# Kernel optimization log

Hardware: AMD Instinct MI355X
Metric: run time of the kernel (lower is better)

## Reference

```python
import jax, jax.numpy as jnp
import numpy as np

NLAYER = 4


def setup_inputs() -> dict:
    key = jax.random.key(0)
    k1, k2, k3 = jax.random.split(key, 3)
    B, T, D, H, L = 32, 512, 512, 512, NLAYER
    scale = 1.0 / np.sqrt(H)
    inputs = jax.random.normal(k1, (B, T, D), dtype=jnp.float32)
    W = jax.random.normal(k2, (L, 3, H, H), dtype=jnp.float32) * scale
    U = jax.random.normal(k3, (L, 3, D, H), dtype=jnp.float32) * scale
    return {"inputs": inputs, "W": W, "U": U}


def _gru_stack(inputs, W, U):
    # inputs: [B, T, D]; W: [L, 3, H, H]; U: [L, 3, D, H]
    L = W.shape[0]
    H = W.shape[-1]
    B = inputs.shape[0]
    x_tbd = jnp.transpose(inputs, (1, 0, 2))  # [T, B, D]
    init = jnp.zeros((L, B, H), dtype=inputs.dtype)

    def step(prev, xt):
        inp = xt
        new_states = []
        for i in range(L):
            z = jax.nn.sigmoid(inp @ U[i, 0] + prev[i] @ W[i, 0])
            r = jax.nn.sigmoid(inp @ U[i, 1] + prev[i] @ W[i, 1])
            h = jnp.tanh(inp @ U[i, 2] + (r * prev[i]) @ W[i, 2])
            s = (1.0 - z) * h + z * prev[i]
            inp = s
            new_states.append(s)
        new = jnp.stack(new_states)  # [L, B, H]
        return new, new_states[-1]  # emit top-layer state

    _, ys = jax.lax.scan(step, init, x_tbd)  # ys: [T, B, H]
    return jnp.transpose(ys, (1, 0, 2))  # [B, T, H]


def reference(inputs, W, U):
    return _gru_stack(inputs, W, U)
```

## Files before the change

### kernel.cpp

```cpp
#include <hip/hip_runtime.h>

#define BB 32
#define TT 512
#define DD 512
#define HH 512
#define LL 4
#define HB (HH * BB)
#define NWG 224
#define TPB 256

#define STATE_FLOATS (LL * 2 * HB)
#define GATE_FLOATS  (3 * LL * HB)
#define DATA_FLOATS  (STATE_FLOATS + GATE_FLOATS)
#define FLAG_STRIDE  64
#define NFLAG        209
#define FLAGS_BYTES  ((unsigned long long)NFLAG * FLAG_STRIDE * 4ull)
#define WS_NEED_BYTES ((unsigned long long)DATA_FLOATS * 4ull + FLAGS_BYTES)

#define KC    64
#define NCH   (HH / KC)
#define IBR   68
#define IBF   (BB * IBR)
#define WLDS  32768
#define LDS_BYTES ((WLDS + 2 * IBF) * 4)

#define DONE_A(f, i) ((f) + (i) * FLAG_STRIDE)
#define DONE_B(f, i) ((f) + (8 + (i)) * FLAG_STRIDE)
#define SPIN_CAP (1 << 22)

__device__ __forceinline__ void wg_wait(int* cnt, int target, int& dead) {
    if (threadIdx.x == 0 && !dead) {
        int spins = 0;
        while (__hip_atomic_load(cnt, __ATOMIC_RELAXED,
                                 __HIP_MEMORY_SCOPE_AGENT) < target) {
            __builtin_amdgcn_s_sleep(2);
            if (++spins > SPIN_CAP) { dead = 1; break; }
        }
        (void)__hip_atomic_load(cnt, __ATOMIC_ACQUIRE,
                                __HIP_MEMORY_SCOPE_AGENT);
    }
    __syncthreads();
}

__device__ __forceinline__ void wg_post(int* cnt) {
    asm volatile("" ::: "memory");
    __builtin_amdgcn_s_waitcnt(0);
    __syncthreads();
    if (threadIdx.x == 0)
        atomicAdd(cnt, 1);
}

__device__ __forceinline__ void pub_store(float* p, float v) {
    __hip_atomic_store(p, v, __ATOMIC_RELAXED, __HIP_MEMORY_SCOPE_AGENT);
}
__device__ __forceinline__ float sigf(float v) {
    return 1.0f / (1.0f + __expf(-v));
}

#define FMA32(WV, E0, E1, E2, E3, E4, E5, E6, E7)                           \
    acc[0][0] = fmaf(E0, WV.x, acc[0][0]); acc[0][1] = fmaf(E0, WV.y, acc[0][1]); \
    acc[0][2] = fmaf(E0, WV.z, acc[0][2]); acc[0][3] = fmaf(E0, WV.w, acc[0][3]); \
    acc[1][0] = fmaf(E1, WV.x, acc[1][0]); acc[1][1] = fmaf(E1, WV.y, acc[1][1]); \
    acc[1][2] = fmaf(E1, WV.z, acc[1][2]); acc[1][3] = fmaf(E1, WV.w, acc[1][3]); \
    acc[2][0] = fmaf(E2, WV.x, acc[2][0]); acc[2][1] = fmaf(E2, WV.y, acc[2][1]); \
    acc[2][2] = fmaf(E2, WV.z, acc[2][2]); acc[2][3] = fmaf(E2, WV.w, acc[2][3]); \
    acc[3][0] = fmaf(E3, WV.x, acc[3][0]); acc[3][1] = fmaf(E3, WV.y, acc[3][1]); \
    acc[3][2] = fmaf(E3, WV.z, acc[3][2]); acc[3][3] = fmaf(E3, WV.w, acc[3][3]); \
    acc[4][0] = fmaf(E4, WV.x, acc[4][0]); acc[4][1] = fmaf(E4, WV.y, acc[4][1]); \
    acc[4][2] = fmaf(E4, WV.z, acc[4][2]); acc[4][3] = fmaf(E4, WV.w, acc[4][3]); \
    acc[5][0] = fmaf(E5, WV.x, acc[5][0]); acc[5][1] = fmaf(E5, WV.y, acc[5][1]); \
    acc[5][2] = fmaf(E5, WV.z, acc[5][2]); acc[5][3] = fmaf(E5, WV.w, acc[5][3]); \
    acc[6][0] = fmaf(E6, WV.x, acc[6][0]); acc[6][1] = fmaf(E6, WV.y, acc[6][1]); \
    acc[6][2] = fmaf(E6, WV.z, acc[6][2]); acc[6][3] = fmaf(E6, WV.w, acc[6][3]); \
    acc[7][0] = fmaf(E7, WV.x, acc[7][0]); acc[7][1] = fmaf(E7, WV.y, acc[7][1]); \
    acc[7][2] = fmaf(E7, WV.z, acc[7][2]); acc[7][3] = fmaf(E7, WV.w, acc[7][3])

#define CHUNK32(RB, WPC)                                                     \
    {                                                                        \
        const float* rbp = (RB) + (bq * 8) * IBR + ksc * 8;                  \
        _Pragma("unroll")                                                    \
        for (int kk = 0; kk < 2; ++kk) {                                     \
            float4 x0 = *(const float4*)&rbp[0 * IBR + kk * 4];              \
            float4 x1 = *(const float4*)&rbp[1 * IBR + kk * 4];              \
            float4 x2 = *(const float4*)&rbp[2 * IBR + kk * 4];              \
            float4 x3 = *(const float4*)&rbp[3 * IBR + kk * 4];              \
            float4 x4 = *(const float4*)&rbp[4 * IBR + kk * 4];              \
            float4 x5 = *(const float4*)&rbp[5 * IBR + kk * 4];              \
            float4 x6 = *(const float4*)&rbp[6 * IBR + kk * 4];              \
            float4 x7 = *(const float4*)&rbp[7 * IBR + kk * 4];              \
            _Pragma("unroll")                                                \
            for (int j = 0; j < 4; ++j) {                                    \
                float4 wv = *(const float4*)&(WPC)[(kk * 4 + j) * 32];       \
                FMA32(wv, (&x0.x)[j], (&x1.x)[j], (&x2.x)[j], (&x3.x)[j],    \
                          (&x4.x)[j], (&x5.x)[j], (&x6.x)[j], (&x7.x)[j]);   \
            }                                                                \
        }                                                                    \
    }

#define REDUCE_SELECT8()                                                     \
    _Pragma("unroll")                                                        \
    for (int i = 0; i < 8; ++i)                                              \
        _Pragma("unroll")                                                    \
        for (int j = 0; j < 4; ++j) {                                        \
            float v = acc[i][j];                                             \
            v += __shfl_xor(v, 1, 64);                                       \
            v += __shfl_xor(v, 2, 64);                                       \
            v += __shfl_xor(v, 4, 64);                                       \
            acc[i][j] = v;                                                   \
        }                                                                    \
    float s0, s1, s2, s3;                                                    \
    if      (ksc == 0) { s0 = acc[0][0]; s1 = acc[0][1]; s2 = acc[0][2]; s3 = acc[0][3]; } \
    else if (ksc == 1) { s0 = acc[1][0]; s1 = acc[1][1]; s2 = acc[1][2]; s3 = acc[1][3]; } \
    else if (ksc == 2) { s0 = acc[2][0]; s1 = acc[2][1]; s2 = acc[2][2]; s3 = acc[2][3]; } \
    else if (ksc == 3) { s0 = acc[3][0]; s1 = acc[3][1]; s2 = acc[3][2]; s3 = acc[3][3]; } \
    else if (ksc == 4) { s0 = acc[4][0]; s1 = acc[4][1]; s2 = acc[4][2]; s3 = acc[4][3]; } \
    else if (ksc == 5) { s0 = acc[5][0]; s1 = acc[5][1]; s2 = acc[5][2]; s3 = acc[5][3]; } \
    else if (ksc == 6) { s0 = acc[6][0]; s1 = acc[6][1]; s2 = acc[6][2]; s3 = acc[6][3]; } \
    else               { s0 = acc[7][0]; s1 = acc[7][1]; s2 = acc[7][2]; s3 = acc[7][3]; }


__global__ __launch_bounds__(TPB) void gru_wave(
    const float* __restrict__ x,
    const float* __restrict__ Wp,
    const float* __restrict__ Up,
    float* __restrict__ out,
    float* __restrict__ ws)
{
    extern __shared__ float lds[];

    const int bid = blockIdx.x;
    const int wg  = (bid & 7) * 28 + (bid >> 3);
    const int tid = threadIdx.x;
    const int sb  = tid >> 4;
    const int sk  = tid & 15;

    float* state = ws;
    float* zbuf  = state + LL * 2 * HB;
    float* rbuf  = zbuf + LL * HB;
    float* hUbuf = rbuf + LL * HB;
    int*   flags = (int*)(ws + DATA_FLOATS);

    float* ib0 = lds + WLDS;
    float* ib1 = ib0 + IBF;

    const bool isZR = wg < 128;
    const bool isHU = (wg >= 128) && (wg < 160);

    int iA = 0, gA = 0, col0 = 0, iB = 0, col0B = 0;
    if (isZR) { int grp = wg >> 4; iA = grp >> 1; gA = grp & 1; col0 = (wg & 15) * 32; }
    else if (isHU) { int w2 = wg - 128; iA = w2 >> 3; col0 = (w2 & 7) * 64; }
    else { int w3 = wg - 160; iB = w3 >> 4; col0B = (w3 & 15) * 32; }

    if (isZR) {
        const float* Um = Up + (size_t)(iA * 3 + gA) * DD * HH + col0;
        const float* Wm = Wp + (size_t)(iA * 3 + gA) * HH * HH + col0;
        for (int u = tid; u < 4096; u += TPB) {
            int k = u >> 3, cc = u & 7;
            *(float4*)&lds[u * 4]         = *(const float4*)&Um[(size_t)k * HH + cc * 4];
            *(float4*)&lds[16384 + u * 4] = *(const float4*)&Wm[(size_t)k * HH + cc * 4];
        }
    } else if (isHU) {
        const float* Mm = Up + (size_t)(iA * 3 + 2) * DD * HH + col0;
        for (int u = tid; u < 8192; u += TPB) {
            int k = u >> 4, cc = u & 15;
            *(float4*)&lds[u * 4] = *(const float4*)&Mm[(size_t)k * HH + cc * 4];
        }
    } else {
        const float* Mm = Wp + (size_t)(iB * 3 + 2) * HH * HH + col0B;
        for (int u = tid; u < 4096; u += TPB) {
            int k = u >> 3, cc = u & 7;
            *(float4*)&lds[u * 4] = *(const float4*)&Mm[(size_t)k * HH + cc * 4];
        }
    }
    __syncthreads();

    int dead = 0;

    if (isZR) {
        const int ksc = tid & 7, cq = (tid >> 3) & 7, bq = tid >> 6;
        const int colq = col0 + cq * 4;
        const int brow = bq * 8 + ksc;
        float* dst = (gA == 0 ? zbuf : rbuf) + (size_t)iA * HB;
        int* cb_up = (iA > 0) ? DONE_B(flags, iA - 1) : nullptr;
        int* cb_my = DONE_B(flags, iA);
        int* c_my  = DONE_A(flags, iA);
        for (int t = 0; t < TT; ++t) {
            float acc[8][4] = {};
            if (cb_up) wg_wait(cb_up, 16 * (t + 1), dead);
            {
                const float* src; size_t rstr;
                if (iA == 0) {
                    src = x + (size_t)sb * TT * DD + (size_t)t * DD + sk * 4;
                    rstr = (size_t)16 * TT * DD;
                } else {
                    src = state + (size_t)((iA - 1) * 2 + (t & 1)) * HB + sb * HH + sk * 4;
                    rstr = (size_t)16 * HH;
                }
                float4 g0 = *(const float4*)&src[0];
                float4 g1 = *(const float4*)&src[rstr];
                src += KC;
                *(float4*)&ib0[sb * IBR + sk * 4]        = g0;
                *(float4*)&ib0[(sb + 16) * IBR + sk * 4] = g1;
                g0 = *(const float4*)&src[0]; g1 = *(const float4*)&src[rstr]; src += KC;
                __syncthreads();
                float *rb = ib0, *nb = ib1;
                const float* wp0 = lds + (ksc * 64 + cq) * 4;
                for (int c = 0; c < NCH; ++c) {
                    const float* wp = wp0 + c * (KC * 8 * 4);
                    CHUNK32(rb, wp);
                    if (c < NCH - 1) {
                        *(float4*)&nb[sb * IBR + sk * 4]        = g0;
                        *(float4*)&nb[(sb + 16) * IBR + sk * 4] = g1;
                        if (c < NCH - 2) {
                            g0 = *(const float4*)&src[0];
                            g1 = *(const float4*)&src[rstr];
                            src += KC;
                        }
                    }
                    __syncthreads();
                    float* tp = rb; rb = nb; nb = tp;
                }
            }
            wg_wait(cb_my, 16 * t, dead);
            {
                const float* src = state + (size_t)(iA * 2 + ((t + 1) & 1)) * HB
                                 + sb * HH + sk * 4;
                const size_t rstr = (size_t)16 * HH;
                float4 g0 = *(const float4*)&src[0];
                float4 g1 = *(const float4*)&src[rstr];
                src += KC;
                *(float4*)&ib0[sb * IBR + sk * 4]        = g0;
                *(float4*)&ib0[(sb + 16) * IBR + sk * 4] = g1;
                g0 = *(const float4*)&src[0]; g1 = *(const float4*)&src[rstr]; src += KC;
                __syncthreads();
                float *rb = ib0, *nb = ib1;
                const float* wp0 = lds + 16384 + (ksc * 64 + cq) * 4;
                for (int c = 0; c < NCH; ++c) {
                    const float* wp = wp0 + c * (KC * 8 * 4);
                    CHUNK32(rb, wp);
                    if (c < NCH - 1) {
                        *(float4*)&nb[sb * IBR + sk * 4]        = g0;
                        *(float4*)&nb[(sb + 16) * IBR + sk * 4] = g1;
                        if (c < NCH - 2) {
                            g0 = *(const float4*)&src[0];
                            g1 = *(const float4*)&src[rstr];
                            src += KC;
                        }
                    }
                    __syncthreads();
                    float* tp = rb; rb = nb; nb = tp;
                }
            }
            float4 p4 = make_float4(0.f, 0.f, 0.f, 0.f);
            if (gA == 1) {
                const float* prowE = state + (size_t)(iA * 2 + ((t + 1) & 1)) * HB
                                   + (size_t)brow * HH + colq;
                p4 = *(const float4*)prowE;
            }
            REDUCE_SELECT8();
            float* drow = dst + (size_t)brow * HH + colq;
            if (gA == 0) {
                pub_store(&drow[0], sigf(s0));
                pub_store(&drow[1], sigf(s1));
                pub_store(&drow[2], sigf(s2));
                pub_store(&drow[3], sigf(s3));
            } else {
                pub_store(&drow[0], sigf(s0) * p4.x);
                pub_store(&drow[1], sigf(s1) * p4.y);
                pub_store(&drow[2], sigf(s2) * p4.z);
                pub_store(&drow[3], sigf(s3) * p4.w);
            }
            wg_post(c_my);
        }
    } else if (isHU) {
        const int ks2 = tid & 1, cq = (tid >> 1) & 15, bq = tid >> 5;
        const int colq = col0 + cq * 4;
        float* hu = hUbuf + (size_t)iA * HB;
        int* cb_up = (iA > 0) ? DONE_B(flags, iA - 1) : nullptr;
        int* cb_my = DONE_B(flags, iA);
        int* c_my  = DONE_A(flags, iA);
        for (int t = 0; t < TT; ++t) {
            float acc[4][4] = {};
            if (cb_up) wg_wait(cb_up, 16 * (t + 1), dead);
            {
                const float* src; size_t rstr;
                if (iA == 0) {
                    src = x + (size_t)sb * TT * DD + (size_t)t * DD + sk * 4;
                    rstr = (size_t)16 * TT * DD;
                } else {
                    src = state + (size_t)((iA - 1) * 2 + (t & 1)) * HB + sb * HH + sk * 4;
                    rstr = (size_t)16 * HH;
                }
                float4 g0 = *(const float4*)&src[0];
                float4 g1 = *(const float4*)&src[rstr];
                src += KC;
                *(float4*)&ib0[sb * IBR + sk * 4]        = g0;
                *(float4*)&ib0[(sb + 16) * IBR + sk * 4] = g1;
                g0 = *(const float4*)&src[0]; g1 = *(const float4*)&src[rstr]; src += KC;
                __syncthreads();
                float *rb = ib0, *nb = ib1;
                const float* wp0 = lds + (ks2 * 32 * 16 + cq) * 4;
                for (int c = 0; c < NCH; ++c) {
                    const float* r0 = rb + (bq * 4 + 0) * IBR + ks2 * 32;
                    const float* r1 = rb + (bq * 4 + 1) * IBR + ks2 * 32;
                    const float* r2 = rb + (bq * 4 + 2) * IBR + ks2 * 32;
                    const float* r3 = rb + (bq * 4 + 3) * IBR + ks2 * 32;
                    const float* wp = wp0 + c * (KC * 16 * 4);
                    #pragma unroll
                    for (int kk = 0; kk < 8; ++kk) {
                        float4 x0 = *(const float4*)&r0[kk * 4];
                        float4 x1 = *(const float4*)&r1[kk * 4];
                        float4 x2 = *(const float4*)&r2[kk * 4];
                        float4 x3 = *(const float4*)&r3[kk * 4];
                        #pragma unroll
                        for (int j = 0; j < 4; ++j) {
                            float4 wv = *(const float4*)&wp[(kk * 4 + j) * 64];
                            float e0 = (&x0.x)[j], e1 = (&x1.x)[j];
                            float e2 = (&x2.x)[j], e3 = (&x3.x)[j];
                            acc[0][0] = fmaf(e0, wv.x, acc[0][0]); acc[0][1] = fmaf(e0, wv.y, acc[0][1]);
                            acc[0][2] = fmaf(e0, wv.z, acc[0][2]); acc[0][3] = fmaf(e0, wv.w, acc[0][3]);
                            acc[1][0] = fmaf(e1, wv.x, acc[1][0]); acc[1][1] = fmaf(e1, wv.y, acc[1][1]);
                            acc[1][2] = fmaf(e1, wv.z, acc[1][2]); acc[1][3] = fmaf(e1, wv.w, acc[1][3]);
                            acc[2][0] = fmaf(e2, wv.x, acc[2][0]); acc[2][1] = fmaf(e2, wv.y, acc[2][1]);
                            acc[2][2] = fmaf(e2, wv.z, acc[2][2]); acc[2][3] = fmaf(e2, wv.w, acc[2][3]);
                            acc[3][0] = fmaf(e3, wv.x, acc[3][0]); acc[3][1] = fmaf(e3, wv.y, acc[3][1]);
                            acc[3][2] = fmaf(e3, wv.z, acc[3][2]); acc[3][3] = fmaf(e3, wv.w, acc[3][3]);
                        }
                    }
                    if (c < NCH - 1) {
                        *(float4*)&nb[sb * IBR + sk * 4]        = g0;
                        *(float4*)&nb[(sb + 16) * IBR + sk * 4] = g1;
                        if (c < NCH - 2) {
                            g0 = *(const float4*)&src[0];
                            g1 = *(const float4*)&src[rstr];
                            src += KC;
                        }
                    }
                    __syncthreads();
                    float* tp = rb; rb = nb; nb = tp;
                }
            }
            wg_wait(cb_my, 16 * t, dead);
            #pragma unroll
            for (int i = 0; i < 4; ++i)
                #pragma unroll
                for (int j = 0; j < 4; ++j) {
                    float v = acc[i][j];
                    v += __shfl_xor(v, 1, 64);
                    acc[i][j] = v;
                }
            float r0v[4], r1v[4];
            if (ks2 == 0) {
                r0v[0]=acc[0][0]; r0v[1]=acc[0][1]; r0v[2]=acc[0][2]; r0v[3]=acc[0][3];
                r1v[0]=acc[1][0]; r1v[1]=acc[1][1]; r1v[2]=acc[1][2]; r1v[3]=acc[1][3];
            } else {
                r0v[0]=acc[2][0]; r0v[1]=acc[2][1]; r0v[2]=acc[2][2]; r0v[3]=acc[2][3];
                r1v[0]=acc[3][0]; r1v[1]=acc[3][1]; r1v[2]=acc[3][2]; r1v[3]=acc[3][3];
            }
            const int b0 = bq * 4 + ks2 * 2;
            float* h0 = hu + (size_t)b0 * HH + colq;
            float* h1 = hu + (size_t)(b0 + 1) * HH + colq;
            pub_store(&h0[0], r0v[0]); pub_store(&h0[1], r0v[1]);
            pub_store(&h0[2], r0v[2]); pub_store(&h0[3], r0v[3]);
            pub_store(&h1[0], r1v[0]); pub_store(&h1[1], r1v[1]);
            pub_store(&h1[2], r1v[2]); pub_store(&h1[3], r1v[3]);
            wg_post(c_my);
        }
    } else {
        const int ksc = tid & 7, cq = (tid >> 3) & 7, bq = tid >> 6;
        const int colq = col0B + cq * 4;
        const int brow = bq * 8 + ksc;
        const float* rbase = rbuf + (size_t)iB * HB;
        const float* hu    = hUbuf + (size_t)iB * HB;
        const float* zz    = zbuf + (size_t)iB * HB;
        int* c_my = DONE_B(flags, iB);
        for (int t = 0; t < TT; ++t) {
            wg_wait(DONE_A(flags, iB), 40 * (t + 1), dead);
            const float* prow = state + (size_t)(iB * 2 + ((t + 1) & 1)) * HB;
            float acc[8][4] = {};
            {
                const float* src = rbase + (size_t)sb * HH + sk * 4;
                const size_t rstr = (size_t)16 * HH;
                float4 g0 = *(const float4*)&src[0];
                float4 g1 = *(const float4*)&src[rstr];
                src += KC;
                *(float4*)&ib0[sb * IBR + sk * 4]        = g0;
                *(float4*)&ib0[(sb + 16) * IBR + sk * 4] = g1;
                g0 = *(const float4*)&src[0]; g1 = *(const float4*)&src[rstr]; src += KC;
                __syncthreads();
                float *rb = ib0, *nb = ib1;
                const float* wp0 = lds + (ksc * 64 + cq) * 4;
                for (int c = 0; c < NCH; ++c) {
                    const float* wp = wp0 + c * (KC * 8 * 4);
                    CHUNK32(rb, wp);
                    if (c < NCH - 1) {
                        *(float4*)&nb[sb * IBR + sk * 4]        = g0;
                        *(float4*)&nb[(sb + 16) * IBR + sk * 4] = g1;
                        if (c < NCH - 2) {
                            g0 = *(const float4*)&src[0];
                            g1 = *(const float4*)&src[rstr];
                            src += KC;
                        }
                    }
                    __syncthreads();
                    float* tp = rb; rb = nb; nb = tp;
                }
            }
            if (iB < 3) wg_wait(DONE_A(flags, iB + 1), 40 * t, dead);
            REDUCE_SELECT8();
            float* stNew = state + (size_t)(iB * 2 + (t & 1)) * HB;
            float4 hu4 = *(const float4*)&hu[(size_t)brow * HH + colq];
            float4 zz4 = *(const float4*)&zz[(size_t)brow * HH + colq];
            float4 pv4 = *(const float4*)&prow[(size_t)brow * HH + colq];
            float av[4] = {s0, s1, s2, s3};
            float4 o4;
            #pragma unroll
            for (int j = 0; j < 4; ++j) {
                float h  = tanhf(av[j] + (&hu4.x)[j]);
                float zg = (&zz4.x)[j];
                float s  = zg * ((&pv4.x)[j] - h) + h;
                pub_store(&stNew[(size_t)brow * HH + colq + j], s);
                (&o4.x)[j] = s;
            }
            if (iB == LL - 1)
                *(float4*)&out[((size_t)brow * TT + t) * HH + colq] = o4;
            wg_post(c_my);
        }
    }
}

extern "C" void kernel_launch(void* const* d_in, const int* in_sizes, int n_in,
                              void* d_out, int out_size, void* d_ws, size_t ws_size,
                              hipStream_t stream) {
    const float* x  = (const float*)d_in[0];
    const float* Wp = (const float*)d_in[1];
    const float* Up = (const float*)d_in[2];
    float* out = (float*)d_out;
    float* ws  = (float*)d_ws;

    if (ws_size < WS_NEED_BYTES) {
        hipMemsetAsync(d_out, 0x7e, (size_t)out_size * sizeof(float), stream);
        return;
    }

    hipMemsetAsync(ws, 0, (size_t)STATE_FLOATS * sizeof(float), stream);
    hipMemsetAsync(ws + DATA_FLOATS, 0, FLAGS_BYTES, stream);

    hipLaunchKernelGGL(gru_wave, dim3(NWG), dim3(TPB), LDS_BYTES, stream,
                       x, Wp, Up, out, ws);
    hipError_t err = hipGetLastError();
    if (err != hipSuccess)
        hipMemsetAsync(d_out, 0x7f, (size_t)out_size * sizeof(float), stream);
}
```

Baseline: 11.55 ms.

## Split r-gate into separate U and W workgroups to shorten per-step critical path

New measurement: 12.48 ms. 1.08x slower.

```diff
diff --git a/kernel.cpp b/kernel.cpp
--- a/kernel.cpp
+++ b/kernel.cpp
@@ -6,7 +6,7 @@
 #define HH 512
 #define LL 4
 #define HB (HH * BB)
-#define NWG 224
+#define NWG 256
 #define TPB 256
 
 #define STATE_FLOATS (LL * 2 * HB)
@@ -24,8 +24,10 @@
 #define WLDS  32768
 #define LDS_BYTES ((WLDS + 2 * IBF) * 4)
 
-#define DONE_A(f, i) ((f) + (i) * FLAG_STRIDE)
-#define DONE_B(f, i) ((f) + (8 + (i)) * FLAG_STRIDE)
+#define DONE_A(f, i)  ((f) + (i) * FLAG_STRIDE)
+#define DONE_R(f, i)  ((f) + (4 + (i)) * FLAG_STRIDE)
+#define DONE_B(f, i)  ((f) + (8 + (i)) * FLAG_STRIDE)
+#define DONE_RU(f, i) ((f) + (12 + (i)) * FLAG_STRIDE)
 #define SPIN_CAP (1 << 22)
 
 __device__ __forceinline__ void wg_wait(int* cnt, int target, int& dead) {
@@ -118,6 +120,36 @@
     else if (ksc == 6) { s0 = acc[6][0]; s1 = acc[6][1]; s2 = acc[6][2]; s3 = acc[6][3]; } \
     else               { s0 = acc[7][0]; s1 = acc[7][1]; s2 = acc[7][2]; s3 = acc[7][3]; }
 
+#define STAGED_GEMV32(SRC0, RSTR, WOFF)                                      \
+    {                                                                        \
+        const float* src = (SRC0);                                           \
+        float4 g0 = *(const float4*)&src[0];                                 \
+        float4 g1 = *(const float4*)&src[RSTR];                              \
+        src += KC;                                                           \
+        *(float4*)&ib0[sb * IBR + sk * 4]        = g0;                       \
+        *(float4*)&ib0[(sb + 16) * IBR + sk * 4] = g1;                       \
+        g0 = *(const float4*)&src[0]; g1 = *(const float4*)&src[RSTR];       \
+        src += KC;                                                           \
+        __syncthreads();                                                     \
+        float *rb = ib0, *nb = ib1;                                          \
+        const float* wp0 = lds + (WOFF) + (ksc * 64 + cq) * 4;               \
+        for (int c = 0; c < NCH; ++c) {                                      \
+            const float* wp = wp0 + c * (KC * 8 * 4);                        \
+            CHUNK32(rb, wp);                                                 \
+            if (c < NCH - 1) {                                               \
+                *(float4*)&nb[sb * IBR + sk * 4]        = g0;                 \
+                *(float4*)&nb[(sb + 16) * IBR + sk * 4] = g1;                 \
+                if (c < NCH - 2) {                                           \
+                    g0 = *(const float4*)&src[0];                            \
+                    g1 = *(const float4*)&src[RSTR];                         \
+                    src += KC;                                               \
+                }                                                            \
+            }                                                                \
+            __syncthreads();                                                 \
+            float* tp = rb; rb = nb; nb = tp;                                \
+        }                                                                    \
+    }
+
 
 __global__ __launch_bounds__(TPB) void gru_wave(
     const float* __restrict__ x,
@@ -129,7 +161,7 @@
     extern __shared__ float lds[];
 
     const int bid = blockIdx.x;
-    const int wg  = (bid & 7) * 28 + (bid >> 3);
+    const int wg  = (bid & 7) * 32 + (bid >> 3);
     const int tid = threadIdx.x;
     const int sb  = tid >> 4;
     const int sk  = tid & 15;
@@ -143,30 +175,34 @@
     float* ib0 = lds + WLDS;
     float* ib1 = ib0 + IBF;
 
-    const bool isZR = wg < 128;
-    const bool isHU = (wg >= 128) && (wg < 160);
-
-    int iA = 0, gA = 0, col0 = 0, iB = 0, col0B = 0;
-    if (isZR) { int grp = wg >> 4; iA = grp >> 1; gA = grp & 1; col0 = (wg & 15) * 32; }
-    else if (isHU) { int w2 = wg - 128; iA = w2 >> 3; col0 = (w2 & 7) * 64; }
-    else { int w3 = wg - 160; iB = w3 >> 4; col0B = (w3 & 15) * 32; }
-
-    if (isZR) {
-        const float* Um = Up + (size_t)(iA * 3 + gA) * DD * HH + col0;
-        const float* Wm = Wp + (size_t)(iA * 3 + gA) * HH * HH + col0;
+    const bool isZ  = wg < 64;
+    const bool isRU = (wg >= 64)  && (wg < 96);
+    const bool isRW = (wg >= 96)  && (wg < 160);
+    const bool isHUw = (wg >= 160) && (wg < 192);
+
+    int iL = 0, col0 = 0;
+    if (isZ)       { iL = wg >> 4;                col0 = (wg & 15) * 32; }
+    else if (isRU) { int w = wg - 64;  iL = w >> 3; col0 = (w & 7) * 64; }
+    else if (isRW) { int w = wg - 96;  iL = w >> 4; col0 = (w & 15) * 32; }
+    else if (isHUw){ int w = wg - 160; iL = w >> 3; col0 = (w & 7) * 64; }
+    else           { int w = wg - 192; iL = w >> 4; col0 = (w & 15) * 32; }
+
+    if (isZ) {
+        const float* Um = Up + (size_t)(iL * 3 + 0) * DD * HH + col0;
+        const float* Wm = Wp + (size_t)(iL * 3 + 0) * HH * HH + col0;
         for (int u = tid; u < 4096; u += TPB) {
             int k = u >> 3, cc = u & 7;
             *(float4*)&lds[u * 4]         = *(const float4*)&Um[(size_t)k * HH + cc * 4];
             *(float4*)&lds[16384 + u * 4] = *(const float4*)&Wm[(size_t)k * HH + cc * 4];
         }
-    } else if (isHU) {
-        const float* Mm = Up + (size_t)(iA * 3 + 2) * DD * HH + col0;
+    } else if (isRU || isHUw) {
+        const float* Mm = Up + (size_t)(iL * 3 + (isRU ? 1 : 2)) * DD * HH + col0;
         for (int u = tid; u < 8192; u += TPB) {
             int k = u >> 4, cc = u & 15;
             *(float4*)&lds[u * 4] = *(const float4*)&Mm[(size_t)k * HH + cc * 4];
         }
     } else {
-        const float* Mm = Wp + (size_t)(iB * 3 + 2) * HH * HH + col0B;
+        const float* Mm = Wp + (size_t)(iL * 3 + (isRW ? 1 : 2)) * HH * HH + col0;
         for (int u = tid; u < 4096; u += TPB) {
             int k = u >> 3, cc = u & 7;
             *(float4*)&lds[u * 4] = *(const float4*)&Mm[(size_t)k * HH + cc * 4];
@@ -176,119 +212,52 @@
 
     int dead = 0;
 
-    if (isZR) {
+    if (isZ) {
         const int ksc = tid & 7, cq = (tid >> 3) & 7, bq = tid >> 6;
         const int colq = col0 + cq * 4;
         const int brow = bq * 8 + ksc;
-        float* dst = (gA == 0 ? zbuf : rbuf) + (size_t)iA * HB;
-        int* cb_up = (iA > 0) ? DONE_B(flags, iA - 1) : nullptr;
-        int* cb_my = DONE_B(flags, iA);
-        int* c_my  = DONE_A(flags, iA);
+        float* dst = zbuf + (size_t)iL * HB;
+        int* cb_up = (iL > 0) ? DONE_B(flags, iL - 1) : nullptr;
+        int* cb_my = DONE_B(flags, iL);
+        int* c_my  = DONE_A(flags, iL);
         for (int t = 0; t < TT; ++t) {
             float acc[8][4] = {};
             if (cb_up) wg_wait(cb_up, 16 * (t + 1), dead);
-            {
-                const float* src; size_t rstr;
-                if (iA == 0) {
-                    src = x + (size_t)sb * TT * DD + (size_t)t * DD + sk * 4;
-                    rstr = (size_t)16 * TT * DD;
-                } else {
-                    src = state + (size_t)((iA - 1) * 2 + (t & 1)) * HB + sb * HH + sk * 4;
-                    rstr = (size_t)16 * HH;
-                }
-                float4 g0 = *(const float4*)&src[0];
-                float4 g1 = *(const float4*)&src[rstr];
-                src += KC;
-                *(float4*)&ib0[sb * IBR + sk * 4]        = g0;
-                *(float4*)&ib0[(sb + 16) * IBR + sk * 4] = g1;
-                g0 = *(const float4*)&src[0]; g1 = *(const float4*)&src[rstr]; src += KC;
-                __syncthreads();
-                float *rb = ib0, *nb = ib1;
-                const float* wp0 = lds + (ksc * 64 + cq) * 4;
-                for (int c = 0; c < NCH; ++c) {
-                    const float* wp = wp0 + c * (KC * 8 * 4);
-                    CHUNK32(rb, wp);
-                    if (c < NCH - 1) {
-                        *(float4*)&nb[sb * IBR + sk * 4]        = g0;
-                        *(float4*)&nb[(sb + 16) * IBR + sk * 4] = g1;
-                        if (c < NCH - 2) {
-                            g0 = *(const float4*)&src[0];
-                            g1 = *(const float4*)&src[rstr];
-                            src += KC;
-                        }
-                    }
-                    __syncthreads();
-                    float* tp = rb; rb = nb; nb = tp;
-                }
+            if (iL == 0) {
+                STAGED_GEMV32(x + (size_t)sb * TT * DD + (size_t)t * DD + sk * 4,
+                              (size_t)16 * TT * DD, 0);
+            } else {
+                STAGED_GEMV32(state + (size_t)((iL - 1) * 2 + (t & 1)) * HB + sb * HH + sk * 4,
+                              (size_t)16 * HH, 0);
             }
             wg_wait(cb_my, 16 * t, dead);
-            {
-                const float* src = state + (size_t)(iA * 2 + ((t + 1) & 1)) * HB
-                                 + sb * HH + sk * 4;
-                const size_t rstr = (size_t)16 * HH;
-                float4 g0 = *(const float4*)&src[0];
-                float4 g1 = *(const float4*)&src[rstr];
-                src += KC;
-                *(float4*)&ib0[sb * IBR + sk * 4]        = g0;
-                *(float4*)&ib0[(sb + 16) * IBR + sk * 4] = g1;
-                g0 = *(const float4*)&src[0]; g1 = *(const float4*)&src[rstr]; src += KC;
-                __syncthreads();
-                float *rb = ib0, *nb = ib1;
-                const float* wp0 = lds + 16384 + (ksc * 64 + cq) * 4;
-                for (int c = 0; c < NCH; ++c) {
-                    const float* wp = wp0 + c * (KC * 8 * 4);
-                    CHUNK32(rb, wp);
-                    if (c < NCH - 1) {
-                        *(float4*)&nb[sb * IBR + sk * 4]        = g0;
-                        *(float4*)&nb[(sb + 16) * IBR + sk * 4] = g1;
-                        if (c < NCH - 2) {
-                            g0 = *(const float4*)&src[0];
-                            g1 = *(const float4*)&src[rstr];
-                            src += KC;
-                        }
-                    }
-                    __syncthreads();
-                    float* tp = rb; rb = nb; nb = tp;
-                }
-            }
-            float4 p4 = make_float4(0.f, 0.f, 0.f, 0.f);
-            if (gA == 1) {
-                const float* prowE = state + (size_t)(iA * 2 + ((t + 1) & 1)) * HB
-                                   + (size_t)brow * HH + colq;
-                p4 = *(const float4*)prowE;
-            }
+            STAGED_GEMV32(state + (size_t)(iL * 2 + ((t + 1) & 1)) * HB + sb * HH + sk * 4,
+                          (size_t)16 * HH, 16384);
             REDUCE_SELECT8();
             float* drow = dst + (size_t)brow * HH + colq;
-            if (gA == 0) {
-                pub_store(&drow[0], sigf(s0));
-                pub_store(&drow[1], sigf(s1));
-                pub_store(&drow[2], sigf(s2));
-                pub_store(&drow[3], sigf(s3));
-            } else {
-                pub_store(&drow[0], sigf(s0) * p4.x);
-                pub_store(&drow[1], sigf(s1) * p4.y);
-                pub_store(&drow[2], sigf(s2) * p4.z);
-                pub_store(&drow[3], sigf(s3) * p4.w);
-            }
+            pub_store(&drow[0], sigf(s0));
+            pub_store(&drow[1], sigf(s1));
+            pub_store(&drow[2], sigf(s2));
+            pub_store(&drow[3], sigf(s3));
             wg_post(c_my);
         }
-    } else if (isHU) {
+    } else if (isRU) {
         const int ks2 = tid & 1, cq = (tid >> 1) & 15, bq = tid >> 5;
         const int colq = col0 + cq * 4;
-        float* hu = hUbuf + (size_t)iA * HB;
-        int* cb_up = (iA > 0) ? DONE_B(flags, iA - 1) : nullptr;
-        int* cb_my = DONE_B(flags, iA);
-        int* c_my  = DONE_A(flags, iA);
+        float* dst = rbuf + (size_t)iL * HB;
+        int* cb_up = (iL > 0) ? DONE_B(flags, iL - 1) : nullptr;
+        int* cb_my = DONE_B(flags, iL);
+        int* c_my  = DONE_RU(flags, iL);
         for (int t = 0; t < TT; ++t) {
             float acc[4][4] = {};
             if (cb_up) wg_wait(cb_up, 16 * (t + 1), dead);
             {
                 const float* src; size_t rstr;
-                if (iA == 0) {
+                if (iL == 0) {
                     src = x + (size_t)sb * TT * DD + (size_t)t * DD + sk * 4;
                     rstr = (size_t)16 * TT * DD;
                 } else {
-                    src = state + (size_t)((iA - 1) * 2 + (t & 1)) * HB + sb * HH + sk * 4;
+                    src = state + (size_t)((iL - 1) * 2 + (t & 1)) * HB + sb * HH + sk * 4;
                     rstr = (size_t)16 * HH;
                 }
                 float4 g0 = *(const float4*)&src[0];
@@ -358,29 +327,56 @@
                 r1v[0]=acc[3][0]; r1v[1]=acc[3][1]; r1v[2]=acc[3][2]; r1v[3]=acc[3][3];
             }
             const int b0 = bq * 4 + ks2 * 2;
-            float* h0 = hu + (size_t)b0 * HH + colq;
-            float* h1 = hu + (size_t)(b0 + 1) * HH + colq;
+            float* h0 = dst + (size_t)b0 * HH + colq;
+            float* h1 = dst + (size_t)(b0 + 1) * HH + colq;
             pub_store(&h0[0], r0v[0]); pub_store(&h0[1], r0v[1]);
             pub_store(&h0[2], r0v[2]); pub_store(&h0[3], r0v[3]);
             pub_store(&h1[0], r1v[0]); pub_store(&h1[1], r1v[1]);
             pub_store(&h1[2], r1v[2]); pub_store(&h1[3], r1v[3]);
             wg_post(c_my);
         }
-    } else {
+    } else if (isRW) {
         const int ksc = tid & 7, cq = (tid >> 3) & 7, bq = tid >> 6;
-        const int colq = col0B + cq * 4;
+        const int colq = col0 + cq * 4;
         const int brow = bq * 8 + ksc;
-        const float* rbase = rbuf + (size_t)iB * HB;
-        const float* hu    = hUbuf + (size_t)iB * HB;
-        const float* zz    = zbuf + (size_t)iB * HB;
-        int* c_my = DONE_B(flags, iB);
+        float* rbase = rbuf + (size_t)iL * HB;
+        int* cb_my = DONE_B(flags, iL);
+        int* c_my  = DONE_R(flags, iL);
         for (int t = 0; t < TT; ++t) {
-            wg_wait(DONE_A(flags, iB), 40 * (t + 1), dead);
-            const float* prow = state + (size_t)(iB * 2 + ((t + 1) & 1)) * HB;
             float acc[8][4] = {};
+            wg_wait(cb_my, 16 * t, dead);
+            const float* prow = state + (size_t)(iL * 2 + ((t + 1) & 1)) * HB;
+            STAGED_GEMV32(prow + sb * HH + sk * 4, (size_t)16 * HH, 0);
+            wg_wait(DONE_RU(flags, iL), 8 * (t + 1), dead);
+            float4 pu4 = *(const float4*)&rbase[(size_t)brow * HH + colq];
+            float4 p4  = *(const float4*)&prow[(size_t)brow * HH + colq];
+            REDUCE_SELECT8();
+            float* drow = rbase + (size_t)brow * HH + colq;
+            pub_store(&drow[0], sigf(s0 + pu4.x) * p4.x);
+            pub_store(&drow[1], sigf(s1 + pu4.y) * p4.y);
+            pub_store(&drow[2], sigf(s2 + pu4.z) * p4.z);
+            pub_store(&drow[3], sigf(s3 + pu4.w) * p4.w);
+            wg_post(c_my);
+        }
+    } else if (isHUw) {
+        const int ks2 = tid & 1, cq = (tid >> 1) & 15, bq = tid >> 5;
+        const int colq = col0 + cq * 4;
+        float* hu = hUbuf + (size_t)iL * HB;
+        int* cb_up = (iL > 0) ? DONE_B(flags, iL - 1) : nullptr;
+        int* cb_my = DONE_B(flags, iL);
+        int* c_my  = DONE_A(flags, iL);
+        for (int t = 0; t < TT; ++t) {
+            float acc[4][4] = {};
+            if (cb_up) wg_wait(cb_up, 16 * (t + 1), dead);
             {
-                const float* src = rbase + (size_t)sb * HH + sk * 4;
-                const size_t rstr = (size_t)16 * HH;
+                const float* src; size_t rstr;
+                if (iL == 0) {
+                    src = x + (size_t)sb * TT * DD + (size_t)t * DD + sk * 4;
+                    rstr = (size_t)16 * TT * DD;
+                } else {
+                    src = state + (size_t)((iL - 1) * 2 + (t & 1)) * HB + sb * HH + sk * 4;
+                    rstr = (size_t)16 * HH;
+                }
                 float4 g0 = *(const float4*)&src[0];
                 float4 g1 = *(const float4*)&src[rstr];
                 src += KC;
@@ -389,10 +385,34 @@
                 g0 = *(const float4*)&src[0]; g1 = *(const float4*)&src[rstr]; src += KC;
                 __syncthreads();
                 float *rb = ib0, *nb = ib1;
-                const float* wp0 = lds + (ksc * 64 + cq) * 4;
+                const float* wp0 = lds + (ks2 * 32 * 16 + cq) * 4;
                 for (int c = 0; c < NCH; ++c) {
-                    const float* wp = wp0 + c * (KC * 8 * 4);
-                    CHUNK32(rb, wp);
+                    const float* r0 = rb + (bq * 4 + 0) * IBR + ks2 * 32;
+                    const float* r1 = rb + (bq * 4 + 1) * IBR + ks2 * 32;
+                    const float* r2 = rb + (bq * 4 + 2) * IBR + ks2 * 32;
+                    const float* r3 = rb + (bq * 4 + 3) * IBR + ks2 * 32;
+                    const float* wp = wp0 + c * (KC * 16 * 4);
+                    #pragma unroll
+                    for (int kk = 0; kk < 8; ++kk) {
+                        float4 x0 = *(const float4*)&r0[kk * 4];
+                        float4 x1 = *(const float4*)&r1[kk * 4];
+                        float4 x2 = *(const float4*)&r2[kk * 4];
+                        float4 x3 = *(const float4*)&r3[kk * 4];
+                        #pragma unroll
+                        for (int j = 0; j < 4; ++j) {
+                            float4 wv = *(const float4*)&wp[(kk * 4 + j) * 64];
+                            float e0 = (&x0.x)[j], e1 = (&x1.x)[j];
+                            float e2 = (&x2.x)[j], e3 = (&x3.x)[j];
+                            acc[0][0] = fmaf(e0, wv.x, acc[0][0]); acc[0][1] = fmaf(e0, wv.y, acc[0][1]);
+                            acc[0][2] = fmaf(e0, wv.z, acc[0][2]); acc[0][3] = fmaf(e0, wv.w, acc[0][3]);
+                            acc[1][0] = fmaf(e1, wv.x, acc[1][0]); acc[1][1] = fmaf(e1, wv.y, acc[1][1]);
+                            acc[1][2] = fmaf(e1, wv.z, acc[1][2]); acc[1][3] = fmaf(e1, wv.w, acc[1][3]);
+                            acc[2][0] = fmaf(e2, wv.x, acc[2][0]); acc[2][1] = fmaf(e2, wv.y, acc[2][1]);
+                            acc[2][2] = fmaf(e2, wv.z, acc[2][2]); acc[2][3] = fmaf(e2, wv.w, acc[2][3]);
+                            acc[3][0] = fmaf(e3, wv.x, acc[3][0]); acc[3][1] = fmaf(e3, wv.y, acc[3][1]);
+                            acc[3][2] = fmaf(e3, wv.z, acc[3][2]); acc[3][3] = fmaf(e3, wv.w, acc[3][3]);
+                        }
+                    }
                     if (c < NCH - 1) {
                         *(float4*)&nb[sb * IBR + sk * 4]        = g0;
                         *(float4*)&nb[(sb + 16) * IBR + sk * 4] = g1;
@@ -406,9 +426,52 @@
                     float* tp = rb; rb = nb; nb = tp;
                 }
             }
-            if (iB < 3) wg_wait(DONE_A(flags, iB + 1), 40 * t, dead);
+            wg_wait(cb_my, 16 * t, dead);
+            #pragma unroll
+            for (int i = 0; i < 4; ++i)
+                #pragma unroll
+                for (int j = 0; j < 4; ++j) {
+                    float v = acc[i][j];
+                    v += __shfl_xor(v, 1, 64);
+                    acc[i][j] = v;
+                }
+            float r0v[4], r1v[4];
+            if (ks2 == 0) {
+                r0v[0]=acc[0][0]; r0v[1]=acc[0][1]; r0v[2]=acc[0][2]; r0v[3]=acc[0][3];
+                r1v[0]=acc[1][0]; r1v[1]=acc[1][1]; r1v[2]=acc[1][2]; r1v[3]=acc[1][3];
+            } else {
+                r0v[0]=acc[2][0]; r0v[1]=acc[2][1]; r0v[2]=acc[2][2]; r0v[3]=acc[2][3];
+                r1v[0]=acc[3][0]; r1v[1]=acc[3][1]; r1v[2]=acc[3][2]; r1v[3]=acc[3][3];
+            }
+            const int b0 = bq * 4 + ks2 * 2;
+            float* h0 = hu + (size_t)b0 * HH + colq;
+            float* h1 = hu + (size_t)(b0 + 1) * HH + colq;
+            pub_store(&h0[0], r0v[0]); pub_store(&h0[1], r0v[1]);
+            pub_store(&h0[2], r0v[2]); pub_store(&h0[3], r0v[3]);
+            pub_store(&h1[0], r1v[0]); pub_store(&h1[1], r1v[1]);
+            pub_store(&h1[2], r1v[2]); pub_store(&h1[3], r1v[3]);
+            wg_post(c_my);
+        }
+    } else {
+        const int ksc = tid & 7, cq = (tid >> 3) & 7, bq = tid >> 6;
+        const int colq = col0 + cq * 4;
+        const int brow = bq * 8 + ksc;
+        const float* rbase = rbuf + (size_t)iL * HB;
+        const float* hu    = hUbuf + (size_t)iL * HB;
+        const float* zz    = zbuf + (size_t)iL * HB;
+        int* c_my = DONE_B(flags, iL);
+        for (int t = 0; t < TT; ++t) {
+            wg_wait(DONE_R(flags, iL), 16 * (t + 1), dead);
+            const float* prow = state + (size_t)(iL * 2 + ((t + 1) & 1)) * HB;
+            float acc[8][4] = {};
+            STAGED_GEMV32(rbase + (size_t)sb * HH + sk * 4, (size_t)16 * HH, 0);
+            wg_wait(DONE_A(flags, iL), 24 * (t + 1), dead);
+            if (iL < 3) {
+                wg_wait(DONE_A(flags, iL + 1), 24 * t, dead);
+                wg_wait(DONE_RU(flags, iL + 1), 8 * t, dead);
+            }
             REDUCE_SELECT8();
-            float* stNew = state + (size_t)(iB * 2 + (t & 1)) * HB;
+            float* stNew = state + (size_t)(iL * 2 + (t & 1)) * HB;
             float4 hu4 = *(const float4*)&hu[(size_t)brow * HH + colq];
             float4 zz4 = *(const float4*)&zz[(size_t)brow * HH + colq];
             float4 pv4 = *(const float4*)&prow[(size_t)brow * HH + colq];
@@ -422,7 +485,7 @@
                 pub_store(&stNew[(size_t)brow * HH + colq + j], s);
                 (&o4.x)[j] = s;
             }
-            if (iB == LL - 1)
+            if (iL == LL - 1)
                 *(float4*)&out[((size_t)brow * TT + t) * HH + colq] = o4;
             wg_post(c_my);
         }
```

## Split hU workgroups to 32 columns each and deepen input prefetch to two chunks

Applied to the files above, without the earlier changes.

New measurement: 11.83 ms. 2.4% more time.

```diff
diff --git a/kernel.cpp b/kernel.cpp
--- a/kernel.cpp
+++ b/kernel.cpp
@@ -6,7 +6,7 @@
 #define HH 512
 #define LL 4
 #define HB (HH * BB)
-#define NWG 224
+#define NWG 256
 #define TPB 256
 
 #define STATE_FLOATS (LL * 2 * HB)
@@ -118,6 +118,40 @@
     else if (ksc == 6) { s0 = acc[6][0]; s1 = acc[6][1]; s2 = acc[6][2]; s3 = acc[6][3]; } \
     else               { s0 = acc[7][0]; s1 = acc[7][1]; s2 = acc[7][2]; s3 = acc[7][3]; }
 
+#define STAGED_GEMV32(SRC0, RSTR, WOFF)                                      \
+    {                                                                        \
+        const float* src = (SRC0);                                           \
+        float4 a0 = *(const float4*)&src[0];                                 \
+        float4 a1 = *(const float4*)&src[RSTR];                              \
+        src += KC;                                                           \
+        *(float4*)&ib0[sb * IBR + sk * 4]        = a0;                       \
+        *(float4*)&ib0[(sb + 16) * IBR + sk * 4] = a1;                       \
+        a0 = *(const float4*)&src[0]; a1 = *(const float4*)&src[RSTR];       \
+        src += KC;                                                           \
+        float4 b0 = *(const float4*)&src[0];                                 \
+        float4 b1 = *(const float4*)&src[RSTR];                              \
+        src += KC;                                                           \
+        __syncthreads();                                                     \
+        float *rb = ib0, *nb = ib1;                                          \
+        const float* wp0 = lds + (WOFF) + (ksc * 64 + cq) * 4;               \
+        for (int c = 0; c < NCH; ++c) {                                      \
+            const float* wp = wp0 + c * (KC * 8 * 4);                        \
+            CHUNK32(rb, wp);                                                 \
+            if (c < NCH - 1) {                                               \
+                *(float4*)&nb[sb * IBR + sk * 4]        = a0;                 \
+                *(float4*)&nb[(sb + 16) * IBR + sk * 4] = a1;                 \
+                a0 = b0; a1 = b1;                                            \
+                if (c < NCH - 3) {                                           \
+                    b0 = *(const float4*)&src[0];                            \
+                    b1 = *(const float4*)&src[RSTR];                         \
+                    src += KC;                                               \
+                }                                                            \
+            }                                                                \
+            __syncthreads();                                                 \
+            float* tp = rb; rb = nb; nb = tp;                                \
+        }                                                                    \
+    }
+
 
 __global__ __launch_bounds__(TPB) void gru_wave(
     const float* __restrict__ x,
@@ -129,7 +163,7 @@
     extern __shared__ float lds[];
 
     const int bid = blockIdx.x;
-    const int wg  = (bid & 7) * 28 + (bid >> 3);
+    const int wg  = (bid & 7) * 32 + (bid >> 3);
     const int tid = threadIdx.x;
     const int sb  = tid >> 4;
     const int sk  = tid & 15;
@@ -144,12 +178,12 @@
     float* ib1 = ib0 + IBF;
 
     const bool isZR = wg < 128;
-    const bool isHU = (wg >= 128) && (wg < 160);
+    const bool isHU = (wg >= 128) && (wg < 192);
 
     int iA = 0, gA = 0, col0 = 0, iB = 0, col0B = 0;
     if (isZR) { int grp = wg >> 4; iA = grp >> 1; gA = grp & 1; col0 = (wg & 15) * 32; }
-    else if (isHU) { int w2 = wg - 128; iA = w2 >> 3; col0 = (w2 & 7) * 64; }
-    else { int w3 = wg - 160; iB = w3 >> 4; col0B = (w3 & 15) * 32; }
+    else if (isHU) { int w2 = wg - 128; iA = w2 >> 4; col0 = (w2 & 15) * 32; }
+    else { int w3 = wg - 192; iB = w3 >> 4; col0B = (w3 & 15) * 32; }
 
     if (isZR) {
         const float* Um = Up + (size_t)(iA * 3 + gA) * DD * HH + col0;
@@ -159,14 +193,9 @@
             *(float4*)&lds[u * 4]         = *(const float4*)&Um[(size_t)k * HH + cc * 4];
             *(float4*)&lds[16384 + u * 4] = *(const float4*)&Wm[(size_t)k * HH + cc * 4];
         }
-    } else if (isHU) {
-        const float* Mm = Up + (size_t)(iA * 3 + 2) * DD * HH + col0;
-        for (int u = tid; u < 8192; u += TPB) {
-            int k = u >> 4, cc = u & 15;
-            *(float4*)&lds[u * 4] = *(const float4*)&Mm[(size_t)k * HH + cc * 4];
-        }
     } else {
-        const float* Mm = Wp + (size_t)(iB * 3 + 2) * HH * HH + col0B;
+        const float* Mm = isHU ? (Up + (size_t)(iA * 3 + 2) * DD * HH + col0)
+                               : (Wp + (size_t)(iB * 3 + 2) * HH * HH + col0B);
         for (int u = tid; u < 4096; u += TPB) {
             int k = u >> 3, cc = u & 7;
             *(float4*)&lds[u * 4] = *(const float4*)&Mm[(size_t)k * HH + cc * 4];
@@ -175,9 +204,9 @@
     __syncthreads();
 
     int dead = 0;
+    const int ksc = tid & 7, cq = (tid >> 3) & 7, bq = tid >> 6;
 
     if (isZR) {
-        const int ksc = tid & 7, cq = (tid >> 3) & 7, bq = tid >> 6;
         const int colq = col0 + cq * 4;
         const int brow = bq * 8 + ksc;
         float* dst = (gA == 0 ? zbuf : rbuf) + (size_t)iA * HB;
@@ -187,70 +216,16 @@
         for (int t = 0; t < TT; ++t) {
             float acc[8][4] = {};
             if (cb_up) wg_wait(cb_up, 16 * (t + 1), dead);
-            {
-                const float* src; size_t rstr;
-                if (iA == 0) {
-                    src = x + (size_t)sb * TT * DD + (size_t)t * DD + sk * 4;
-                    rstr = (size_t)16 * TT * DD;
-                } else {
-                    src = state + (size_t)((iA - 1) * 2 + (t & 1)) * HB + sb * HH + sk * 4;
-                    rstr = (size_t)16 * HH;
-                }
-                float4 g0 = *(const float4*)&src[0];
-                float4 g1 = *(const float4*)&src[rstr];
-                src += KC;
-                *(float4*)&ib0[sb * IBR + sk * 4]        = g0;
-                *(float4*)&ib0[(sb + 16) * IBR + sk * 4] = g1;
-                g0 = *(const float4*)&src[0]; g1 = *(const float4*)&src[rstr]; src += KC;
-                __syncthreads();
-                float *rb = ib0, *nb = ib1;
-                const float* wp0 = lds + (ksc * 64 + cq) * 4;
-                for (int c = 0; c < NCH; ++c) {
-                    const float* wp = wp0 + c * (KC * 8 * 4);
-                    CHUNK32(rb, wp);
-                    if (c < NCH - 1) {
-                        *(float4*)&nb[sb * IBR + sk * 4]        = g0;
-                        *(float4*)&nb[(sb + 16) * IBR + sk * 4] = g1;
-                        if (c < NCH - 2) {
-                            g0 = *(const float4*)&src[0];
-                            g1 = *(const float4*)&src[rstr];
-                            src += KC;
-                        }
-                    }
-                    __syncthreads();
-                    float* tp = rb; rb = nb; nb = tp;
-                }
+            if (iA == 0) {
+                STAGED_GEMV32(x + (size_t)sb * TT * DD + (size_t)t * DD + sk * 4,
+                              (size_t)16 * TT * DD, 0);
+            } else {
+                STAGED_GEMV32(state + (size_t)((iA - 1) * 2 + (t & 1)) * HB + sb * HH + sk * 4,
+                              (size_t)16 * HH, 0);
             }
             wg_wait(cb_my, 16 * t, dead);
-            {
-                const float* src = state + (size_t)(iA * 2 + ((t + 1) & 1)) * HB
-                                 + sb * HH + sk * 4;
-                const size_t rstr = (size_t)16 * HH;
-                float4 g0 = *(const float4*)&src[0];
-                float4 g1 = *(const float4*)&src[rstr];
-                src += KC;
-                *(float4*)&ib0[sb * IBR + sk * 4]        = g0;
-                *(float4*)&ib0[(sb + 16) * IBR + sk * 4] = g1;
-                g0 = *(const float4*)&src[0]; g1 = *(const float4*)&src[rstr]; src += KC;
-                __syncthreads();
-                float *rb = ib0, *nb = ib1;
-                const float* wp0 = lds + 16384 + (ksc * 64 + cq) * 4;
-                for (int c = 0; c < NCH; ++c) {
-                    const float* wp = wp0 + c * (KC * 8 * 4);
-                    CHUNK32(rb, wp);
-                    if (c < NCH - 1) {
-                        *(float4*)&nb[sb * IBR + sk * 4]        = g0;
-                        *(float4*)&nb[(sb + 16) * IBR + sk * 4] = g1;
-                        if (c < NCH - 2) {
-                            g0 = *(const float4*)&src[0];
-                            g1 = *(const float4*)&src[rstr];
-                            src += KC;
-                        }
-                    }
-                    __syncthreads();
-                    float* tp = rb; rb = nb; nb = tp;
-                }
-            }
+            STAGED_GEMV32(state + (size_t)(iA * 2 + ((t + 1) & 1)) * HB + sb * HH + sk * 4,
+                          (size_t)16 * HH, 16384);
             float4 p4 = make_float4(0.f, 0.f, 0.f, 0.f);
             if (gA == 1) {
                 const float* prowE = state + (size_t)(iA * 2 + ((t + 1) & 1)) * HB
@@ -273,101 +248,32 @@
             wg_post(c_my);
         }
     } else if (isHU) {
-        const int ks2 = tid & 1, cq = (tid >> 1) & 15, bq = tid >> 5;
         const int colq = col0 + cq * 4;
+        const int brow = bq * 8 + ksc;
         float* hu = hUbuf + (size_t)iA * HB;
         int* cb_up = (iA > 0) ? DONE_B(flags, iA - 1) : nullptr;
         int* cb_my = DONE_B(flags, iA);
         int* c_my  = DONE_A(flags, iA);
         for (int t = 0; t < TT; ++t) {
-            float acc[4][4] = {};
+            float acc[8][4] = {};
             if (cb_up) wg_wait(cb_up, 16 * (t + 1), dead);
-            {
-                const float* src; size_t rstr;
-                if (iA == 0) {
-                    src = x + (size_t)sb * TT * DD + (size_t)t * DD + sk * 4;
-                    rstr = (size_t)16 * TT * DD;
-                } else {
-                    src = state + (size_t)((iA - 1) * 2 + (t & 1)) * HB + sb * HH + sk * 4;
-                    rstr = (size_t)16 * HH;
-                }
-                float4 g0 = *(const float4*)&src[0];
-                float4 g1 = *(const float4*)&src[rstr];
-                src += KC;
-                *(float4*)&ib0[sb * IBR + sk * 4]        = g0;
-                *(float4*)&ib0[(sb + 16) * IBR + sk * 4] = g1;
-                g0 = *(const float4*)&src[0]; g1 = *(const float4*)&src[rstr]; src += KC;
-                __syncthreads();
-                float *rb = ib0, *nb = ib1;
-                const float* wp0 = lds + (ks2 * 32 * 16 + cq) * 4;
-                for (int c = 0; c < NCH; ++c) {
-                    const float* r0 = rb + (bq * 4 + 0) * IBR + ks2 * 32;
-                    const float* r1 = rb + (bq * 4 + 1) * IBR + ks2 * 32;
-                    const float* r2 = rb + (bq * 4 + 2) * IBR + ks2 * 32;
-                    const float* r3 = rb + (bq * 4 + 3) * IBR + ks2 * 32;
-                    const float* wp = wp0 + c * (KC * 16 * 4);
-                    #pragma unroll
-                    for (int kk = 0; kk < 8; ++kk) {
-                        float4 x0 = *(const float4*)&r0[kk * 4];
-                        float4 x1 = *(const float4*)&r1[kk * 4];
-                        float4 x2 = *(const float4*)&r2[kk * 4];
-                        float4 x3 = *(const float4*)&r3[kk * 4];
-                        #pragma unroll
-                        for (int j = 0; j < 4; ++j) {
-                            float4 wv = *(const float4*)&wp[(kk * 4 + j) * 64];
-                            float e0 = (&x0.x)[j], e1 = (&x1.x)[j];
-                            float e2 = (&x2.x)[j], e3 = (&x3.x)[j];
-                            acc[0][0] = fmaf(e0, wv.x, acc[0][0]); acc[0][1] = fmaf(e0, wv.y, acc[0][1]);
-                            acc[0][2] = fmaf(e0, wv.z, acc[0][2]); acc[0][3] = fmaf(e0, wv.w, acc[0][3]);
-                            acc[1][0] = fmaf(e1, wv.x, acc[1][0]); acc[1][1] = fmaf(e1, wv.y, acc[1][1]);
-                            acc[1][2] = fmaf(e1, wv.z, acc[1][2]); acc[1][3] = fmaf(e1, wv.w, acc[1][3]);
-                            acc[2][0] = fmaf(e2, wv.x, acc[2][0]); acc[2][1] = fmaf(e2, wv.y, acc[2][1]);
-                            acc[2][2] = fmaf(e2, wv.z, acc[2][2]); acc[2][3] = fmaf(e2, wv.w, acc[2][3]);
-                            acc[3][0] = fmaf(e3, wv.x, acc[3][0]); acc[3][1] = fmaf(e3, wv.y, acc[3][1]);
-                            acc[3][2] = fmaf(e3, wv.z, acc[3][2]); acc[3][3] = fmaf(e3, wv.w, acc[3][3]);
-                        }
-                    }
-                    if (c < NCH - 1) {
-                        *(float4*)&nb[sb * IBR + sk * 4]        = g0;
-                        *(float4*)&nb[(sb + 16) * IBR + sk * 4] = g1;
-                        if (c < NCH - 2) {
-                            g0 = *(const float4*)&src[0];
-                            g1 = *(const float4*)&src[rstr];
-                            src += KC;
-                        }
-                    }
-                    __syncthreads();
-                    float* tp = rb; rb = nb; nb = tp;
-                }
+            if (iA == 0) {
+                STAGED_GEMV32(x + (size_t)sb * TT * DD + (size_t)t * DD + sk * 4,
+                              (size_t)16 * TT * DD, 0);
+            } else {
+                STAGED_GEMV32(state + (size_t)((iA - 1) * 2 + (t & 1)) * HB + sb * HH + sk * 4,
+                              (size_t)16 * HH, 0);
             }
             wg_wait(cb_my, 16 * t, dead);
-            #pragma unroll
-            for (int i = 0; i < 4; ++i)
-                #pragma unroll
-                for (int j = 0; j < 4; ++j) {
-                    float v = acc[i][j];
-                    v += __shfl_xor(v, 1, 64);
-                    acc[i][j] = v;
-                }
-            float r0v[4], r1v[4];
-            if (ks2 == 0) {
-                r0v[0]=acc[0][0]; r0v[1]=acc[0][1]; r0v[2]=acc[0][2]; r0v[3]=acc[0][3];
-                r1v[0]=acc[1][0]; r1v[1]=acc[1][1]; r1v[2]=acc[1][2]; r1v[3]=acc[1][3];
-            } else {
-                r0v[0]=acc[2][0]; r0v[1]=acc[2][1]; r0v[2]=acc[2][2]; r0v[3]=acc[2][3];
-                r1v[0]=acc[3][0]; r1v[1]=acc[3][1]; r1v[2]=acc[3][2]; r1v[3]=acc[3][3];
-            }
-            const int b0 = bq * 4 + ks2 * 2;
-            float* h0 = hu + (size_t)b0 * HH + colq;
-            float* h1 = hu + (size_t)(b0 + 1) * HH + colq;
-            pub_store(&h0[0], r0v[0]); pub_store(&h0[1], r0v[1]);
-            pub_store(&h0[2], r0v[2]); pub_store(&h0[3], r0v[3]);
-            pub_store(&h1[0], r1v[0]); pub_store(&h1[1], r1v[1]);
-            pub_store(&h1[2], r1v[2]); pub_store(&h1[3], r1v[3]);
+            REDUCE_SELECT8();
+            float* drow = hu + (size_t)brow * HH + colq;
+            pub_store(&drow[0], s0);
+            pub_store(&drow[1], s1);
+            pub_store(&drow[2], s2);
+            pub_store(&drow[3], s3);
             wg_post(c_my);
         }
     } else {
-        const int ksc = tid & 7, cq = (tid >> 3) & 7, bq = tid >> 6;
         const int colq = col0B + cq * 4;
         const int brow = bq * 8 + ksc;
         const float* rbase = rbuf + (size_t)iB * HB;
@@ -375,38 +281,11 @@
         const float* zz    = zbuf + (size_t)iB * HB;
         int* c_my = DONE_B(flags, iB);
         for (int t = 0; t < TT; ++t) {
-            wg_wait(DONE_A(flags, iB), 40 * (t + 1), dead);
+            wg_wait(DONE_A(flags, iB), 48 * (t + 1), dead);
             const float* prow = state + (size_t)(iB * 2 + ((t + 1) & 1)) * HB;
             float acc[8][4] = {};
-            {
-                const float* src = rbase + (size_t)sb * HH + sk * 4;
-                const size_t rstr = (size_t)16 * HH;
-                float4 g0 = *(const float4*)&src[0];
-                float4 g1 = *(const float4*)&src[rstr];
-                src += KC;
-                *(float4*)&ib0[sb * IBR + sk * 4]        = g0;
-                *(float4*)&ib0[(sb + 16) * IBR + sk * 4] = g1;
-                g0 = *(const float4*)&src[0]; g1 = *(const float4*)&src[rstr]; src += KC;
-                __syncthreads();
-                float *rb = ib0, *nb = ib1;
-                const float* wp0 = lds + (ksc * 64 + cq) * 4;
-                for (int c = 0; c < NCH; ++c) {
-                    const float* wp = wp0 + c * (KC * 8 * 4);
-                    CHUNK32(rb, wp);
-                    if (c < NCH - 1) {
-                        *(float4*)&nb[sb * IBR + sk * 4]        = g0;
-                        *(float4*)&nb[(sb + 16) * IBR + sk * 4] = g1;
-                        if (c < NCH - 2) {
-                            g0 = *(const float4*)&src[0];
-                            g1 = *(const float4*)&src[rstr];
-                            src += KC;
-                        }
-                    }
-                    __syncthreads();
-                    float* tp = rb; rb = nb; nb = tp;
-                }
-            }
-            if (iB < 3) wg_wait(DONE_A(flags, iB + 1), 40 * t, dead);
+            STAGED_GEMV32(rbase + (size_t)sb * HH + sk * 4, (size_t)16 * HH, 0);
+            if (iB < 3) wg_wait(DONE_A(flags, iB + 1), 48 * t, dead);
             REDUCE_SELECT8();
             float* stNew = state + (size_t)(iB * 2 + (t & 1)) * HB;
             float4 hu4 = *(const float4*)&hu[(size_t)brow * HH + colq];
```
